# Kernel tuning notes

Measured on AMD Instinct MI355X. Metric: run time of the kernel, lower is better.

## Reference

```python
import jax, jax.numpy as jnp
import numpy as np

BATCH, N, D, N_STEPS = 16, 128, 128, 5
EPS = 1e-10

def setup_inputs() -> dict:
    key = jax.random.key(0)
    k1, k2 = jax.random.split(key)
    x = jax.random.normal(k1, (BATCH, D), dtype=jnp.float32)
    L = jax.random.normal(k2, (N, D, D), dtype=jnp.float32) * 0.1
    temperature = jnp.array(1.0, dtype=jnp.float32)
    target_similarity = jnp.array(-0.5, dtype=jnp.float32)
    step_size = jnp.array(0.1, dtype=jnp.float32)
    return {"x": x, "L": L, "temperature": temperature,
            "target_similarity": target_similarity, "step_size": step_size}

def _bases(L):
    # Cayley transform per bubble: U = (I + A)^{-1} (I - A), A skew-symmetric
    A = L - jnp.swapaxes(L, -1, -2)               # [N, d, d]
    I = jnp.eye(L.shape[-1], dtype=L.dtype)
    return jnp.linalg.solve(I[None] + A, I[None] - A)  # [N, d, d]

def reference(x, L, temperature, target_similarity, step_size):
    n = L.shape[0]
    bases = _bases(L)                              # [N, d, d]

    # measurements[b, i] = x[b] @ U_i
    measurements = jnp.einsum('bd,ndk->bnk', x, bases)  # [B, N, d]

    # surface tension: pairwise Frobenius distance between bases
    diff_b = bases[None, :] - bases[:, None]       # [N, N, d, d]
    tension = jnp.sqrt(jnp.sum(diff_b ** 2, axis=(-2, -1)) + 1e-8)  # [N, N]

    temp = jnp.maximum(jnp.abs(temperature), 0.01)
    interaction = jax.nn.softmax(-tension / temp, axis=-1)  # [N, N]
    mask = 1.0 - jnp.eye(n, dtype=x.dtype)
    w = (mask * interaction)[None]                 # [1, N, N]
    step = jnp.clip(jnp.abs(step_size), 0.001, 0.5)

    state = measurements
    for _ in range(N_STEPS):
        state_n = state / (jnp.linalg.norm(state, axis=-1, keepdims=True) + EPS)
        cos_sim = jnp.einsum('bnd,bmd->bnm', state_n, state_n)   # [B, N, N]
        force_mag = (cos_sim - target_similarity) * w            # [B, N, N]
        diff = state[:, :, None, :] - state[:, None, :, :]       # [B, N, N, d]
        diff_n = diff / (jnp.linalg.norm(diff, axis=-1, keepdims=True) + EPS)
        forces = jnp.einsum('bnm,bnmd->bnd', force_mag, diff_n)  # [B, N, d]
        state = state + step * forces
    equilibrium = state

    # expressions[b, i] = equilibrium[b, i] @ U_i^T
    expressions = jnp.einsum('bnd,nkd->bnk', equilibrium, bases)

    # density matrix per batch element
    m_norm = equilibrium / (jnp.linalg.norm(equilibrium, axis=-1, keepdims=True) + EPS)
    rho = jnp.einsum('bnd,bne->bde', m_norm, m_norm) / n         # [B, d, d]
    eigenvalues = jnp.linalg.eigvalsh(rho)                        # [B, d]
    eigenvalues = jnp.maximum(eigenvalues, 1e-12)
    output_dist = eigenvalues / jnp.sum(eigenvalues, axis=-1, keepdims=True)

    output_avg = jnp.mean(expressions, axis=1)                   # [B, d]
    return (output_avg, output_dist, rho, measurements, equilibrium,
            expressions, tension)
```

## Files before the change

### kernel.cpp

```cpp
#include <hip/hip_runtime.h>

#define EPSF 1e-10f

__device__ __forceinline__ float f4sel(float4 a, int cc) {
  float r = (cc == 0) ? a.x : a.y;
  r = (cc == 2) ? a.z : r;
  r = (cc == 3) ? a.w : r;
  return r;
}

__device__ __forceinline__ float dpp_pair_sum(float x) {
  return x + __int_as_float(__builtin_amdgcn_update_dpp(
      0, __float_as_int(x), 0xB1, 0xf, 0xf, true));
}

__device__ __forceinline__ float dpp_red_sum64(float x) {
  x += __int_as_float(__builtin_amdgcn_update_dpp(0, __float_as_int(x), 0x111, 0xf, 0xf, true));
  x += __int_as_float(__builtin_amdgcn_update_dpp(0, __float_as_int(x), 0x112, 0xf, 0xf, true));
  x += __int_as_float(__builtin_amdgcn_update_dpp(0, __float_as_int(x), 0x114, 0xf, 0xe, true));
  x += __int_as_float(__builtin_amdgcn_update_dpp(0, __float_as_int(x), 0x118, 0xf, 0xc, true));
  x += __int_as_float(__builtin_amdgcn_update_dpp(0, __float_as_int(x), 0x142, 0xa, 0xf, true));
  x += __int_as_float(__builtin_amdgcn_update_dpp(0, __float_as_int(x), 0x143, 0xc, 0xf, true));
  return __int_as_float(__builtin_amdgcn_readlane(__float_as_int(x), 63));
}

#define SWZ4(i, j4) ((i) * 32 + ((j4) ^ ((i) & 31)))
#define SWZF(i, j) (SWZ4((i), (j) >> 2) * 4 + ((j) & 3))

__global__ __launch_bounds__(512, 2) void k_cayley(const float* __restrict__ L,
                                                   float* __restrict__ bases) {
  extern __shared__ float4 sm4[];
  float4* M4  = sm4;
  float*  Mf  = (float*)M4;
  float4* rb0 = sm4 + 4096;
  float4* rb1 = rb0 + 32;
  float*  cb0 = (float*)(rb1 + 32);
  float*  cb1 = cb0 + 128;
  const int n = blockIdx.x, t = threadIdx.x;
  const float* Ln = L + n * 16384;
  for (int f = t; f < 4096; f += 512) {
    int i = f >> 5, j4 = f & 31;
    M4[SWZ4(i, j4)] = ((const float4*)Ln)[f];
  }
  __syncthreads();
  for (int f = t; f < 16384; f += 512) {
    int i = f >> 7, j = f & 127;
    if (i < j) {
      int a = SWZF(i, j), b = SWZF(j, i);
      float va = Mf[a], vb = Mf[b];
      Mf[a] = va - vb;
      Mf[b] = vb - va;
    } else if (i == j) {
      Mf[SWZF(i, i)] = 1.0f;
    }
  }
  __syncthreads();
  const int i = t & 127;
  const int h2 = t >> 7;
  float4 Ar[8];
  #pragma unroll
  for (int u = 0; u < 8; ++u) Ar[u] = M4[SWZ4(i, h2 * 8 + u)];
  if (i == 0) {
    #pragma unroll
    for (int u = 0; u < 8; ++u) rb0[h2 * 8 + u] = Ar[u];
  }
  if (h2 == 0) cb0[i] = Ar[0].x;
  __syncthreads();
  for (int k = 0; k < 128; ++k) {
    const float4* rbC = (k & 1) ? rb1 : rb0;
    float4*       rbN = (k & 1) ? rb0 : rb1;
    const float*  cbC = (k & 1) ? cb1 : cb0;
    float*        cbN = (k & 1) ? cb0 : cb1;
    const float pivinv = 1.0f / cbC[k];
    const float coef = cbC[i] * pivinv;
    const int kj4 = k >> 2, kc = k & 3;
    const int nj4 = (k + 1) >> 2, ncc = (k + 1) & 3;
    const bool isPiv = (i == k);
    const bool isNext = (i == k + 1);
    float colv = 0.0f;
    #pragma unroll
    for (int u = 0; u < 8; ++u) {
      const int jj = h2 * 8 + u;
      float4 r = rbC[jj];
      float4 a;
      if (isPiv) {
        a.x = r.x * pivinv; a.y = r.y * pivinv;
        a.z = r.z * pivinv; a.w = r.w * pivinv;
        if (jj == kj4) {
          a.x = (kc == 0) ? pivinv : a.x;
          a.y = (kc == 1) ? pivinv : a.y;
          a.z = (kc == 2) ? pivinv : a.z;
          a.w = (kc == 3) ? pivinv : a.w;
        }
      } else {
        a = Ar[u];
        a.x -= coef * r.x; a.y -= coef * r.y;
        a.z -= coef * r.z; a.w -= coef * r.w;
        if (jj == kj4) {
          a.x = (kc == 0) ? -coef : a.x;
          a.y = (kc == 1) ? -coef : a.y;
          a.z = (kc == 2) ? -coef : a.z;
          a.w = (kc == 3) ? -coef : a.w;
        }
      }
      Ar[u] = a;
      if (jj == nj4) colv = f4sel(a, ncc);
      if (isNext) rbN[jj] = a;
    }
    if (h2 == (nj4 >> 3)) cbN[i] = colv;
    __syncthreads();
  }
  #pragma unroll
  for (int u = 0; u < 8; ++u) M4[SWZ4(i, h2 * 8 + u)] = Ar[u];
  __syncthreads();
  for (int f = t; f < 16384; f += 512) {
    int ii = f >> 7, j = f & 127;
    float v = Mf[SWZF(ii, j)];
    bases[n * 16384 + f] = 2.0f * v - ((ii == j) ? 1.0f : 0.0f);
  }
}

__global__ __launch_bounds__(256) void k_gramp(const float* __restrict__ bases,
                                               float* __restrict__ part) {
  __shared__ __align__(16) float tile[64][132];
  const int b = blockIdx.x, t = threadIdx.x;
  const int tx = t & 15, ty = t >> 4;
  const int i0 = tx * 8, j0 = ty * 8;
  const int k0 = b * 512;
  float acc[8][8];
  #pragma unroll
  for (int u = 0; u < 8; ++u)
    #pragma unroll
    for (int v = 0; v < 8; ++v) acc[u][v] = 0.f;
  for (int c0 = 0; c0 < 512; c0 += 64) {
    __syncthreads();
    for (int f = t; f < 8192; f += 256) {
      int i = f >> 6, kk = f & 63;
      tile[kk][i] = bases[i * 16384 + k0 + c0 + kk];
    }
    __syncthreads();
    for (int kk = 0; kk < 64; ++kk) {
      float4 a0 = *(const float4*)&tile[kk][i0];
      float4 a1 = *(const float4*)&tile[kk][i0 + 4];
      float4 b0 = *(const float4*)&tile[kk][j0];
      float4 b1 = *(const float4*)&tile[kk][j0 + 4];
      float av[8] = {a0.x, a0.y, a0.z, a0.w, a1.x, a1.y, a1.z, a1.w};
      float bv[8] = {b0.x, b0.y, b0.z, b0.w, b1.x, b1.y, b1.z, b1.w};
      #pragma unroll
      for (int u = 0; u < 8; ++u)
        #pragma unroll
        for (int v = 0; v < 8; ++v) acc[u][v] += av[u] * bv[v];
    }
  }
  float* P = part + b * 16384;
  #pragma unroll
  for (int u = 0; u < 8; ++u) {
    #pragma unroll
    for (int v4 = 0; v4 < 2; ++v4) {
      float4 o;
      o.x = acc[u][v4 * 4 + 0]; o.y = acc[u][v4 * 4 + 1];
      o.z = acc[u][v4 * 4 + 2]; o.w = acc[u][v4 * 4 + 3];
      *(float4*)&P[(i0 + u) * 128 + j0 + v4 * 4] = o;
    }
  }
}

__global__ __launch_bounds__(256) void k_gsum(const float* __restrict__ part,
                                              float* __restrict__ G) {
  const int g = blockIdx.x * 256 + threadIdx.x;
  float s = 0.f;
  for (int p = 0; p < 32; ++p) s += part[p * 16384 + g];
  G[g] = s;
}

__global__ __launch_bounds__(128) void k_wsoft(const float* __restrict__ G,
                                               const float* __restrict__ temp_p,
                                               float* __restrict__ w,
                                               float* __restrict__ tension_out) {
  const int i = blockIdx.x, t = threadIdx.x;
  __shared__ float rr[2], r2[2];
  float temp = fmaxf(fabsf(*temp_p), 0.01f);
  float gii = G[i * 128 + i], gjj = G[t * 128 + t], gij = G[i * 128 + t];
  float ten = sqrtf(fmaxf(gii + gjj - 2.0f * gij, 0.0f) + 1e-8f);
  tension_out[i * 128 + t] = ten;
  float logit = -ten / temp;
  float m = logit;
  for (int s = 32; s > 0; s >>= 1) m = fmaxf(m, __shfl_xor(m, s));
  if ((t & 63) == 0) rr[t >> 6] = m;
  __syncthreads();
  float mx = fmaxf(rr[0], rr[1]);
  float ex = expf(logit - mx);
  float ssum = ex;
  for (int s = 32; s > 0; s >>= 1) ssum += __shfl_xor(ssum, s);
  if ((t & 63) == 0) r2[t >> 6] = ssum;
  __syncthreads();
  float tot = r2[0] + r2[1];
  float wv = ex / tot;
  if (t == i) wv = 0.0f;
  w[i * 128 + t] = wv;
}

__global__ __launch_bounds__(128) void k_meas(const float* __restrict__ x,
                                              const float* __restrict__ bases,
                                              float* __restrict__ meas_out,
                                              float* __restrict__ state0,
                                              float* __restrict__ norms0) {
  const int n = blockIdx.x, t = threadIdx.x;
  __shared__ float xs[2048];
  __shared__ float red[2];
  for (int f = t; f < 2048; f += 128) xs[f] = x[f];
  __syncthreads();
  float acc[16];
  #pragma unroll
  for (int b = 0; b < 16; ++b) acc[b] = 0.f;
  for (int d = 0; d < 128; ++d) {
    float u = bases[n * 16384 + d * 128 + t];
    #pragma unroll
    for (int b = 0; b < 16; ++b) acc[b] += xs[b * 128 + d] * u;
  }
  for (int b = 0; b < 16; ++b) {
    meas_out[(b * 128 + n) * 128 + t] = acc[b];
    state0[(b * 128 + n) * 128 + t] = acc[b];
  }
  for (int b = 0; b < 16; ++b) {
    float v = acc[b] * acc[b];
    for (int s = 32; s > 0; s >>= 1) v += __shfl_down(v, s);
    if ((t & 63) == 0) red[t >> 6] = v;
    __syncthreads();
    if (t == 0) norms0[b * 128 + n] = sqrtf(red[0] + red[1]);
    __syncthreads();
  }
}

__global__ __launch_bounds__(128) void k_step(const float* __restrict__ src,
                                              float* __restrict__ dst,
                                              const float* __restrict__ w,
                                              const float* __restrict__ norms_in,
                                              float* __restrict__ norms_out,
                                              const float* __restrict__ tgt_p,
                                              const float* __restrict__ step_p) {
  const int b = blockIdx.x >> 7, n = blockIdx.x & 127, t = threadIdx.x;
  __shared__ float sn[128];
  __shared__ __align__(16) float chunk[32][132];
  __shared__ float red[2][32][2];
  __shared__ float cbuf[32];
  __shared__ float red2[2];
  const float target = *tgt_p;
  const float step = fminf(fmaxf(fabsf(*step_p), 0.001f), 0.5f);
  const float* srcb = src + b * 16384;
  float x_d = srcb[n * 128 + t];
  sn[t] = x_d;
  float norm_n = norms_in[b * 128 + n];
  float f_d = 0.0f;
  __syncthreads();
  for (int c0 = 0; c0 < 128; c0 += 32) {
    for (int f = t; f < 1024; f += 128) {
      int row = f >> 5, c4 = f & 31;
      ((float4*)&chunk[row][0])[c4] =
          ((const float4*)(srcb + (c0 + row) * 128))[c4];
    }
    __syncthreads();
    int m = t & 31, q = t >> 5;
    float dp = 0.f, sp = 0.f;
    const float* cr = &chunk[m][0];
    #pragma unroll
    for (int i2 = 0; i2 < 32; ++i2) {
      int dd = q * 32 + i2;
      float smv = cr[dd];
      float snd = sn[dd];
      dp += smv * snd;
      float df = snd - smv;
      sp += df * df;
    }
    dp += __shfl_xor(dp, 32);
    sp += __shfl_xor(sp, 32);
    int wave = t >> 6;
    if ((t & 63) < 32) { red[wave][m][0] = dp; red[wave][m][1] = sp; }
    __syncthreads();
    if (t < 32) {
      float dot = red[0][t][0] + red[1][t][0];
      float sq  = red[0][t][1] + red[1][t][1];
      int mm = c0 + t;
      float norm_m = norms_in[b * 128 + mm];
      float wnm = w[n * 128 + mm];
      float cs = dot / ((norm_n + EPSF) * (norm_m + EPSF));
      float fm = (cs - target) * wnm;
      cbuf[t] = fm / (sqrtf(fmaxf(sq, 0.0f)) + EPSF);
    }
    __syncthreads();
    #pragma unroll
    for (int mi = 0; mi < 32; ++mi) f_d += cbuf[mi] * (x_d - chunk[mi][t]);
    __syncthreads();
  }
  float nv = x_d + step * f_d;
  dst[(b * 128 + n) * 128 + t] = nv;
  float v = nv * nv;
  for (int s = 32; s > 0; s >>= 1) v += __shfl_down(v, s);
  if ((t & 63) == 0) red2[t >> 6] = v;
  __syncthreads();
  if (t == 0) norms_out[b * 128 + n] = sqrtf(red2[0] + red2[1]);
}

__global__ __launch_bounds__(128) void k_expr(const float* __restrict__ eq,
                                              const float* __restrict__ bases,
                                              float* __restrict__ expr_out) {
  const int n = blockIdx.x, t = threadIdx.x;
  __shared__ __align__(16) float es[16][128];
  for (int f = t; f < 2048; f += 128)
    es[f >> 7][f & 127] = eq[((f >> 7) * 128 + n) * 128 + (f & 127)];
  __syncthreads();
  float acc[16];
  #pragma unroll
  for (int b = 0; b < 16; ++b) acc[b] = 0.f;
  const float4* U = (const float4*)(bases + n * 16384 + t * 128);
  for (int d4 = 0; d4 < 32; ++d4) {
    float4 u = U[d4];
    #pragma unroll
    for (int b = 0; b < 16; ++b) {
      float4 e4 = ((const float4*)&es[b][0])[d4];
      acc[b] += u.x * e4.x + u.y * e4.y + u.z * e4.z + u.w * e4.w;
    }
  }
  for (int b = 0; b < 16; ++b) expr_out[(b * 128 + n) * 128 + t] = acc[b];
}

__global__ __launch_bounds__(128) void k_avg(const float* __restrict__ expr,
                                             float* __restrict__ avg) {
  const int b = blockIdx.x, t = threadIdx.x;
  float s = 0.f;
  for (int n = 0; n < 128; ++n) s += expr[(b * 128 + n) * 128 + t];
  avg[b * 128 + t] = s * (1.0f / 128.0f);
}

__global__ __launch_bounds__(256) void k_rho(const float* __restrict__ eq,
                                             const float* __restrict__ norms,
                                             float* __restrict__ rho) {
  const int b = blockIdx.x >> 3, dt = blockIdx.x & 7;
  const int t = threadIdx.x;
  __shared__ float ch[32][129];
  int e = t & 127, dl = t >> 7;
  float acc[8];
  #pragma unroll
  for (int o = 0; o < 8; ++o) acc[o] = 0.f;
  for (int c0 = 0; c0 < 128; c0 += 32) {
    for (int f = t; f < 4096; f += 256) {
      int row = f >> 7, col = f & 127;
      int nn = c0 + row;
      float inv = 1.0f / (norms[b * 128 + nn] + EPSF);
      ch[row][col] = eq[(b * 128 + nn) * 128 + col] * inv;
    }
    __syncthreads();
    for (int nn = 0; nn < 32; ++nn) {
      float me = ch[nn][e];
      #pragma unroll
      for (int o = 0; o < 8; ++o) {
        int d = dt * 16 + dl + o * 2;
        acc[o] += ch[nn][d] * me;
      }
    }
    __syncthreads();
  }
  for (int o = 0; o < 8; ++o) {
    int d = dt * 16 + dl + o * 2;
    rho[(b * 128 + d) * 128 + e] = acc[o] * (1.0f / 128.0f);
  }
}

__global__ __launch_bounds__(256, 1) void k_tridiag(const float* __restrict__ rho,
                                                    float* __restrict__ dvec_g,
                                                    float* __restrict__ evec_g) {
  __shared__ __align__(16) float cb0[128];
  __shared__ __align__(16) float cb1[128];
  __shared__ __align__(16) float pbuf[128];
  __shared__ float dvl[128], evl[128];
  __shared__ float redS[4], redK[4], redX[1];
  const int bb = blockIdx.x, t = threadIdx.x;
  const int i = t >> 1, h = t & 1, wv = t >> 6;
  const float* R = rho + bb * 16384;
  float4 Ar[16];
  const float4* Rp = (const float4*)(R + i * 128 + h * 64);
  #pragma unroll
  for (int u = 0; u < 16; ++u) Ar[u] = Rp[u];
  if (h == 0) {
    cb0[i] = (i == 0) ? 0.f : Ar[0].x;
    if (i == 0) dvl[0] = Ar[0].x;
    if (i == 1) redX[0] = Ar[0].x;
  }
  {
    float s2w = dpp_red_sum64((h == 0 && i > 0) ? Ar[0].x * Ar[0].x : 0.f);
    if ((t & 63) == 0) redS[wv] = s2w;
  }
  __syncthreads();
  for (int k = 0; k < 126; ++k) {
    const float* cbC = (k & 1) ? cb1 : cb0;
    float*       cbN = (k & 1) ? cb0 : cb1;
    float sig2 = redS[0] + redS[1] + redS[2] + redS[3];
    float x0 = redX[0];
    const bool skip = (sig2 < 1e-30f);
    float sig = sqrtf(sig2);
    float alpha = (x0 >= 0.f) ? -sig : sig;
    if (skip) alpha = 0.f;
    float beta = skip ? 0.f : 1.f / (sig2 - alpha * x0);
    float w0 = x0 - alpha;
    if (t == 0) evl[k] = alpha;
    const int jn4 = (k + 1) >> 2, ncc = (k + 1) & 3, hn = (k + 1) >> 6;
    float vt = (i == k + 1) ? w0 : cbC[i];
    const float4* cv4 = (const float4*)cbC;
    float pp = 0.f;
    #pragma unroll
    for (int u = 0; u < 16; ++u) {
      const int jj = h * 16 + u;
      float4 v = cv4[jj];
      if (jj == jn4) {
        v.x = (0 == ncc) ? w0 : v.x;
        v.y = (1 == ncc) ? w0 : v.y;
        v.z = (2 == ncc) ? w0 : v.z;
        v.w = (3 == ncc) ? w0 : v.w;
      }
      pp += Ar[u].x * v.x + Ar[u].y * v.y + Ar[u].z * v.z + Ar[u].w * v.w;
    }
    pp = dpp_pair_sum(pp);
    float p = beta * pp;
    if (i <= k) p = 0.f;
    if (h == 0) pbuf[i] = p;
    float kpw = dpp_red_sum64((h == 0) ? vt * p : 0.f);
    if ((t & 63) == 0) redK[wv] = kpw;
    __syncthreads();
    float K = (redK[0] + redK[1] + redK[2] + redK[3]) * beta * 0.5f;
    float cn = 0.f;
    if (i > k) {
      float qt = p - K * vt;
      const float4* pv4 = (const float4*)pbuf;
      #pragma unroll
      for (int u = 0; u < 16; ++u) {
        const int jj = h * 16 + u;
        float4 v = cv4[jj];
        if (jj == jn4) {
          v.x = (0 == ncc) ? w0 : v.x;
          v.y = (1 == ncc) ? w0 : v.y;
          v.z = (2 == ncc) ? w0 : v.z;
          v.w = (3 == ncc) ? w0 : v.w;
        }
        float4 pq = pv4[jj];
        float qx = pq.x - K * v.x, qy = pq.y - K * v.y;
        float qz = pq.z - K * v.z, qw = pq.w - K * v.w;
        Ar[u].x -= vt * qx + qt * v.x;
        Ar[u].y -= vt * qy + qt * v.y;
        Ar[u].z -= vt * qz + qt * v.z;
        Ar[u].w -= vt * qw + qt * v.w;
        if (jj == jn4) cn = f4sel(Ar[u], ncc);
      }
    }
    if (h == hn) cbN[i] = (i <= k + 1) ? 0.f : cn;
    if (i == k + 1 && h == hn) dvl[k + 1] = cn;
    if (i == k + 2 && h == hn) redX[0] = cn;
    float s2w = dpp_red_sum64((h == hn && i > k + 1) ? cn * cn : 0.f);
    if ((t & 63) == 0) redS[wv] = s2w;
    __syncthreads();
  }
  if (i == 126 && h == 1) dvl[126] = Ar[15].z;
  if (i == 127 && h == 1) { evl[126] = Ar[15].z; dvl[127] = Ar[15].w; }
  if (t == 0) evl[127] = 0.0f;
  __syncthreads();
  if (t < 128) {
    dvec_g[bb * 128 + t] = dvl[t];
    evec_g[bb * 128 + t] = evl[t];
  }
}

__global__ __launch_bounds__(1024, 1) void k_bisect(const float* __restrict__ dvec_g,
                                                    const float* __restrict__ evec_g,
                                                    float* __restrict__ dist_out) {
  const int bb = blockIdx.x, t = threadIdx.x;
  const int idx = t >> 3;
  const int c = t & 7;
  __shared__ float ds[128], e2s[128], eabs[128];
  __shared__ float lam[128];
  __shared__ float rr[2];
  if (t < 128) {
    ds[t] = dvec_g[bb * 128 + t];
    float e = evec_g[bb * 128 + t];
    e2s[t] = e * e;
    eabs[t] = fabsf(e);
  }
  __syncthreads();
  float lo = 1e30f, hi = -1e30f;
  for (int ii = 0; ii < 128; ++ii) {
    float r = (ii > 0 ? eabs[ii - 1] : 0.0f) + (ii < 127 ? eabs[ii] : 0.0f);
    lo = fminf(lo, ds[ii] - r);
    hi = fmaxf(hi, ds[ii] + r);
  }
  const float frac = (float)(c + 1) * (1.0f / 9.0f);
  for (int it = 0; it < 13; ++it) {
    float mid = lo + (hi - lo) * frac;
    int cnt = 0;
    float q = ds[0] - mid;
    if (q < 0.0f) cnt++;
    for (int ii = 1; ii < 128; ++ii) {
      float denom = q;
      if (fabsf(denom) < 1e-25f) denom = (denom < 0.0f) ? -1e-25f : 1e-25f;
      q = (ds[ii] - mid) - __fdividef(e2s[ii - 1], denom);
      if (q < 0.0f) cnt++;
    }
    bool isLo = (cnt <= idx);
    float cl = isLo ? mid : -1e30f;
    float ch = isLo ? 1e30f : mid;
    #pragma unroll
    for (int s = 1; s < 8; s <<= 1) {
      cl = fmaxf(cl, __shfl_xor(cl, s));
      ch = fminf(ch, __shfl_xor(ch, s));
    }
    lo = fmaxf(lo, cl);
    hi = fminf(hi, ch);
  }
  if (c == 0) lam[idx] = 0.5f * (lo + hi);
  __syncthreads();
  if (t < 128) {
    float evc = fmaxf(lam[t], 1e-12f);
    float ssum = evc;
    for (int s = 32; s > 0; s >>= 1) ssum += __shfl_xor(ssum, s);
    if ((t & 63) == 0) rr[t >> 6] = ssum;
    __syncthreads();
    float tot = rr[0] + rr[1];
    dist_out[bb * 128 + t] = evc / tot;
  } else {
    __syncthreads();
  }
}

extern "C" void kernel_launch(void* const* d_in, const int* in_sizes, int n_in,
                              void* d_out, int out_size, void* d_ws, size_t ws_size,
                              hipStream_t stream) {
  const float* x      = (const float*)d_in[0];
  const float* L      = (const float*)d_in[1];
  const float* temp_p = (const float*)d_in[2];
  const float* tgt_p  = (const float*)d_in[3];
  const float* step_p = (const float*)d_in[4];
  float* out = (float*)d_out;
  float* ws  = (float*)d_ws;

  float* bases = ws;
  float* G     = bases + 2097152;
  float* w     = G + 16384;
  float* s0    = w + 16384;
  float* s1    = s0 + 262144;
  float* n0    = s1 + 262144;
  float* n1    = n0 + 2048;
  float* dv    = n1 + 2048;
  float* ev    = dv + 2048;

  float* gpart = s0;

  float* o_avg  = out;
  float* o_dist = out + 2048;
  float* o_rho  = out + 4096;
  float* o_meas = out + 266240;
  float* o_eq   = out + 528384;
  float* o_expr = out + 790528;
  float* o_ten  = out + 1052672;

  hipFuncSetAttribute((const void*)k_cayley,
                      hipFuncAttributeMaxDynamicSharedMemorySize, 67584);

  k_cayley<<<128, 512, 67584, stream>>>(L, bases);
  k_gramp<<<32, 256, 0, stream>>>(bases, gpart);
  k_gsum<<<64, 256, 0, stream>>>(gpart, G);
  k_wsoft<<<128, 128, 0, stream>>>(G, temp_p, w, o_ten);
  k_meas<<<128, 128, 0, stream>>>(x, bases, o_meas, s0, n0);
  k_step<<<2048, 128, 0, stream>>>(s0, s1, w, n0, n1, tgt_p, step_p);
  k_step<<<2048, 128, 0, stream>>>(s1, s0, w, n1, n0, tgt_p, step_p);
  k_step<<<2048, 128, 0, stream>>>(s0, s1, w, n0, n1, tgt_p, step_p);
  k_step<<<2048, 128, 0, stream>>>(s1, s0, w, n1, n0, tgt_p, step_p);
  k_step<<<2048, 128, 0, stream>>>(s0, o_eq, w, n0, n1, tgt_p, step_p);
  k_expr<<<128, 128, 0, stream>>>(o_eq, bases, o_expr);
  k_avg<<<16, 128, 0, stream>>>(o_expr, o_avg);
  k_rho<<<128, 256, 0, stream>>>(o_eq, n1, o_rho);
  k_tridiag<<<16, 256, 0, stream>>>(o_rho, dv, ev);
  k_bisect<<<16, 1024, 0, stream>>>(dv, ev, o_dist);
}
```

Measured before the change: 914.3 us.

## Widen tridiagonalization to four threads per row; derive pair distance from dot product

```diff
diff --git a/kernel.cpp b/kernel.cpp
--- a/kernel.cpp
+++ b/kernel.cpp
@@ -9,9 +9,12 @@
   return r;
 }
 
-__device__ __forceinline__ float dpp_pair_sum(float x) {
-  return x + __int_as_float(__builtin_amdgcn_update_dpp(
+__device__ __forceinline__ float dpp_quad_sum(float x) {
+  x += __int_as_float(__builtin_amdgcn_update_dpp(
       0, __float_as_int(x), 0xB1, 0xf, 0xf, true));
+  x += __int_as_float(__builtin_amdgcn_update_dpp(
+      0, __float_as_int(x), 0x4E, 0xf, 0xf, true));
+  return x;
 }
 
 __device__ __forceinline__ float dpp_red_sum64(float x) {
@@ -242,7 +245,7 @@
   const int b = blockIdx.x >> 7, n = blockIdx.x & 127, t = threadIdx.x;
   __shared__ float sn[128];
   __shared__ __align__(16) float chunk[32][132];
-  __shared__ float red[2][32][2];
+  __shared__ float red[2][32];
   __shared__ float cbuf[32];
   __shared__ float red2[2];
   const float target = *tgt_p;
@@ -251,6 +254,7 @@
   float x_d = srcb[n * 128 + t];
   sn[t] = x_d;
   float norm_n = norms_in[b * 128 + n];
+  float nn2 = norm_n * norm_n;
   float f_d = 0.0f;
   __syncthreads();
   for (int c0 = 0; c0 < 128; c0 += 32) {
@@ -261,27 +265,22 @@
     }
     __syncthreads();
     int m = t & 31, q = t >> 5;
-    float dp = 0.f, sp = 0.f;
+    float dp = 0.f;
     const float* cr = &chunk[m][0];
     #pragma unroll
     for (int i2 = 0; i2 < 32; ++i2) {
       int dd = q * 32 + i2;
-      float smv = cr[dd];
-      float snd = sn[dd];
-      dp += smv * snd;
-      float df = snd - smv;
-      sp += df * df;
+      dp += cr[dd] * sn[dd];
     }
     dp += __shfl_xor(dp, 32);
-    sp += __shfl_xor(sp, 32);
     int wave = t >> 6;
-    if ((t & 63) < 32) { red[wave][m][0] = dp; red[wave][m][1] = sp; }
+    if ((t & 63) < 32) red[wave][m] = dp;
     __syncthreads();
     if (t < 32) {
-      float dot = red[0][t][0] + red[1][t][0];
-      float sq  = red[0][t][1] + red[1][t][1];
+      float dot = red[0][t] + red[1][t];
       int mm = c0 + t;
       float norm_m = norms_in[b * 128 + mm];
+      float sq = nn2 + norm_m * norm_m - 2.0f * dot;
       float wnm = w[n * 128 + mm];
       float cs = dot / ((norm_n + EPSF) * (norm_m + EPSF));
       float fm = (cs - target) * wnm;
@@ -366,21 +365,21 @@
   }
 }
 
-__global__ __launch_bounds__(256, 1) void k_tridiag(const float* __restrict__ rho,
+__global__ __launch_bounds__(512, 1) void k_tridiag(const float* __restrict__ rho,
                                                     float* __restrict__ dvec_g,
                                                     float* __restrict__ evec_g) {
   __shared__ __align__(16) float cb0[128];
   __shared__ __align__(16) float cb1[128];
   __shared__ __align__(16) float pbuf[128];
   __shared__ float dvl[128], evl[128];
-  __shared__ float redS[4], redK[4], redX[1];
+  __shared__ float redS[8], redK[8], redX[1];
   const int bb = blockIdx.x, t = threadIdx.x;
-  const int i = t >> 1, h = t & 1, wv = t >> 6;
+  const int i = t >> 2, h = t & 3, wv = t >> 6;
   const float* R = rho + bb * 16384;
-  float4 Ar[16];
-  const float4* Rp = (const float4*)(R + i * 128 + h * 64);
-  #pragma unroll
-  for (int u = 0; u < 16; ++u) Ar[u] = Rp[u];
+  float4 Ar[8];
+  const float4* Rp = (const float4*)(R + i * 128 + h * 32);
+  #pragma unroll
+  for (int u = 0; u < 8; ++u) Ar[u] = Rp[u];
   if (h == 0) {
     cb0[i] = (i == 0) ? 0.f : Ar[0].x;
     if (i == 0) dvl[0] = Ar[0].x;
@@ -394,7 +393,8 @@
   for (int k = 0; k < 126; ++k) {
     const float* cbC = (k & 1) ? cb1 : cb0;
     float*       cbN = (k & 1) ? cb0 : cb1;
-    float sig2 = redS[0] + redS[1] + redS[2] + redS[3];
+    float sig2 = redS[0] + redS[1] + redS[2] + redS[3] +
+                 redS[4] + redS[5] + redS[6] + redS[7];
     float x0 = redX[0];
     const bool skip = (sig2 < 1e-30f);
     float sig = sqrtf(sig2);
@@ -403,13 +403,13 @@
     float beta = skip ? 0.f : 1.f / (sig2 - alpha * x0);
     float w0 = x0 - alpha;
     if (t == 0) evl[k] = alpha;
-    const int jn4 = (k + 1) >> 2, ncc = (k + 1) & 3, hn = (k + 1) >> 6;
+    const int jn4 = (k + 1) >> 2, ncc = (k + 1) & 3, hn = (k + 1) >> 5;
     float vt = (i == k + 1) ? w0 : cbC[i];
     const float4* cv4 = (const float4*)cbC;
     float pp = 0.f;
     #pragma unroll
-    for (int u = 0; u < 16; ++u) {
-      const int jj = h * 16 + u;
+    for (int u = 0; u < 8; ++u) {
+      const int jj = h * 8 + u;
       float4 v = cv4[jj];
       if (jj == jn4) {
         v.x = (0 == ncc) ? w0 : v.x;
@@ -419,21 +419,22 @@
       }
       pp += Ar[u].x * v.x + Ar[u].y * v.y + Ar[u].z * v.z + Ar[u].w * v.w;
     }
-    pp = dpp_pair_sum(pp);
+    pp = dpp_quad_sum(pp);
     float p = beta * pp;
     if (i <= k) p = 0.f;
     if (h == 0) pbuf[i] = p;
     float kpw = dpp_red_sum64((h == 0) ? vt * p : 0.f);
     if ((t & 63) == 0) redK[wv] = kpw;
     __syncthreads();
-    float K = (redK[0] + redK[1] + redK[2] + redK[3]) * beta * 0.5f;
+    float K = (redK[0] + redK[1] + redK[2] + redK[3] +
+               redK[4] + redK[5] + redK[6] + redK[7]) * beta * 0.5f;
     float cn = 0.f;
     if (i > k) {
       float qt = p - K * vt;
       const float4* pv4 = (const float4*)pbuf;
       #pragma unroll
-      for (int u = 0; u < 16; ++u) {
-        const int jj = h * 16 + u;
+      for (int u = 0; u < 8; ++u) {
+        const int jj = h * 8 + u;
         float4 v = cv4[jj];
         if (jj == jn4) {
           v.x = (0 == ncc) ? w0 : v.x;
@@ -458,8 +459,8 @@
     if ((t & 63) == 0) redS[wv] = s2w;
     __syncthreads();
   }
-  if (i == 126 && h == 1) dvl[126] = Ar[15].z;
-  if (i == 127 && h == 1) { evl[126] = Ar[15].z; dvl[127] = Ar[15].w; }
+  if (i == 126 && h == 3) dvl[126] = Ar[7].z;
+  if (i == 127 && h == 3) { evl[126] = Ar[7].z; dvl[127] = Ar[7].w; }
   if (t == 0) evl[127] = 0.0f;
   __syncthreads();
   if (t < 128) {
@@ -575,6 +576,6 @@
   k_expr<<<128, 128, 0, stream>>>(o_eq, bases, o_expr);
   k_avg<<<16, 128, 0, stream>>>(o_expr, o_avg);
   k_rho<<<128, 256, 0, stream>>>(o_eq, n1, o_rho);
-  k_tridiag<<<16, 256, 0, stream>>>(o_rho, dv, ev);
+  k_tridiag<<<16, 512, 0, stream>>>(o_rho, dv, ev);
   k_bisect<<<16, 1024, 0, stream>>>(dv, ev, o_dist);
 }
```

Result: faster. 859.1 us (-6.0%).
